# Performance work log

Measured on AMD Instinct MI355X. Metric: run time of the kernel, lower is better.

Reference implementation:

```python
import jax, jax.numpy as jnp
import numpy as np

B, N, C = 8, 8192, 512
H = 8
D = C // H  # 64
EPS = 1e-6


def setup_inputs() -> dict:
    key = jax.random.key(0)
    k1, k2, k3, k4 = jax.random.split(key, 4)
    x = jax.random.normal(k1, (B, N, C), dtype=jnp.float32)
    # nn.Linear(dim, dim*3, bias=False): weight [3C, C]; we store transposed [C, 3C]
    w_qkv = jax.random.normal(k2, (C, 3 * C), dtype=jnp.float32) * (1.0 / np.sqrt(C))
    w_proj = jax.random.normal(k3, (C, C), dtype=jnp.float32) * (1.0 / np.sqrt(C))
    b_proj = jax.random.normal(k4, (C,), dtype=jnp.float32) * 0.01
    return {"x": x, "w_qkv": w_qkv, "w_proj": w_proj, "b_proj": b_proj}


def _linear_attention(q, k, v):
    # q,k,v: [B,H,N,D]; elu+1 feature map, non-causal linear attention
    qf = jax.nn.elu(q) + 1.0
    kf = jax.nn.elu(k) + 1.0
    kv = jnp.einsum('bhnd,bhne->bhde', kf, v)          # [B,H,D,D] state
    z = jnp.einsum('bhnd,bhd->bhn', qf, kf.sum(axis=2))  # normalizer
    out = jnp.einsum('bhnd,bhde->bhne', qf, kv) / (z[..., None] + EPS)
    return out  # [B,H,N,D]


def reference(x, w_qkv, w_proj, b_proj):
    b, n, c = x.shape
    qkv = x @ w_qkv                                   # [B,N,3C]
    qkv = qkv.reshape(b, n, 3, H, D).transpose(2, 0, 3, 1, 4)  # [3,B,H,N,D]
    q, k, v = qkv[0], qkv[1], qkv[2]
    attn = _linear_attention(q, k, v)                 # [B,H,N,D]
    y = attn.transpose(0, 2, 1, 3).reshape(b, n, c)   # [B,N,C]
    return y @ w_proj + b_proj
```

## Files before the change

kernel.cpp:

```cpp
#include <hip/hip_runtime.h>
#include <cstdint>
#include <cstddef>

#define BDIM 8
#define NSEQ 8192
#define CDIM 512
#define HEADS 8
#define HD 64
#define NSPLIT 16

typedef short bf16x8 __attribute__((ext_vector_type(8)));
typedef float f32x4 __attribute__((ext_vector_type(4)));

typedef const __attribute__((address_space(1))) void* gas_cvp;
typedef __attribute__((address_space(3))) void* las_vp;

__device__ __forceinline__ void gload_lds16(const void* g, void* l) {
    __builtin_amdgcn_global_load_lds((gas_cvp)g, (las_vp)l, 16, 0, 0);
}

__device__ __forceinline__ ushort f2bf_rne(float f) {
    uint32_t u = __float_as_uint(f);
    u += 0x7FFFu + ((u >> 16) & 1u);
    return (ushort)(u >> 16);
}
__device__ __forceinline__ float bf2f(ushort h) {
    return __uint_as_float(((uint32_t)h) << 16);
}

__device__ __forceinline__ void split8(const float4 p0, const float4 p1,
                                       bf16x8& hi, bf16x8& lo) {
    const float xs[8] = {p0.x, p0.y, p0.z, p0.w, p1.x, p1.y, p1.z, p1.w};
#pragma unroll
    for (int e = 0; e < 8; ++e) {
        const uint32_t u = __float_as_uint(xs[e]);
        const ushort h = (ushort)(u >> 16);
        const float r = xs[e] - __uint_as_float((uint32_t)h << 16);
        hi[e] = (short)h;
        lo[e] = (short)(__float_as_uint(r) >> 16);
    }
}

__device__ __forceinline__ float elu1(float x) {
    return x > 0.f ? x + 1.f : __expf(x);
}

__global__ __launch_bounds__(256)
void split_wT_kernel(const float* __restrict__ W, ushort* __restrict__ WTh,
                     ushort* __restrict__ WTl, int N) {
    __shared__ float tile[32][33];
    const int tx = threadIdx.x & 31, ty = threadIdx.x >> 5;
    const int bx = blockIdx.x, by = blockIdx.y;
#pragma unroll
    for (int r = 0; r < 4; ++r)
        tile[ty + 8 * r][tx] = W[(size_t)(by * 32 + ty + 8 * r) * N + bx * 32 + tx];
    __syncthreads();
#pragma unroll
    for (int r = 0; r < 4; ++r) {
        const int n = bx * 32 + ty + 8 * r;
        const int k = by * 32 + tx;
        const float v = tile[tx][ty + 8 * r];
        const ushort h = f2bf_rne(v);
        WTh[(size_t)n * 512 + k] = h;
        WTl[(size_t)n * 512 + k] = f2bf_rne(v - bf2f(h));
    }
}

__global__ __launch_bounds__(256, 2)
void qkv_mfma_kernel(const float* __restrict__ X,
                     const ushort* __restrict__ BTh, const ushort* __restrict__ BTl,
                     float* __restrict__ qf, float* __restrict__ kf, float* __restrict__ v) {
    __shared__ __align__(16) char lds[32768];
    const int t = threadIdx.x, l = t & 63, w = t >> 6;
    const int wm = w >> 1, wn = w & 1;
    const int bid = blockIdx.x;
    const int swz = (bid & 7) * 768 + (bid >> 3);
    const int brow = swz / 12, bcol = swz % 12;

    const int f0 = 2 * w, f1 = 2 * w + 1;
    const ushort* gb0 = BTh + (size_t)(bcol * 128 + f0 * 16 + (l & 15)) * 512 + ((l >> 4) * 8);
    const ushort* gb1 = BTh + (size_t)(bcol * 128 + f1 * 16 + (l & 15)) * 512 + ((l >> 4) * 8);
    const ushort* gb2 = BTl + (size_t)(bcol * 128 + f0 * 16 + (l & 15)) * 512 + ((l >> 4) * 8);
    const ushort* gb3 = BTl + (size_t)(bcol * 128 + f1 * 16 + (l & 15)) * 512 + ((l >> 4) * 8);

    const float* gA = X + (size_t)(brow * 128 + wm * 64 + (l & 15)) * 512 + ((l >> 4) * 8);

    f32x4 acc[4][4];
    const f32x4 zero = {0.f, 0.f, 0.f, 0.f};
#pragma unroll
    for (int i = 0; i < 4; ++i)
#pragma unroll
        for (int j = 0; j < 4; ++j) acc[i][j] = zero;

    auto stage = [&](int buf, int kt) {
        char* Ld = lds + buf * 16384;
        gload_lds16(gb0 + kt, Ld + 0 * 8192 + f0 * 1024);
        gload_lds16(gb1 + kt, Ld + 0 * 8192 + f1 * 1024);
        gload_lds16(gb2 + kt, Ld + 1 * 8192 + f0 * 1024);
        gload_lds16(gb3 + kt, Ld + 1 * 8192 + f1 * 1024);
    };

    stage(0, 0);
    __syncthreads();
    int cur = 0;
    for (int ks = 0; ks < 16; ++ks) {
        const int kt = ks * 32;
        if (ks < 15) stage(cur ^ 1, kt + 32);
        bf16x8 ah[4], al[4];
#pragma unroll
        for (int i = 0; i < 4; ++i) {
            const float* pa = gA + (size_t)i * 16 * 512 + kt;
            const float4 p0 = *(const float4*)(pa);
            const float4 p1 = *(const float4*)(pa + 4);
            split8(p0, p1, ah[i], al[i]);
        }
        const char* Lb = lds + cur * 16384;
        bf16x8 bh[4], bl[4];
#pragma unroll
        for (int j = 0; j < 4; ++j) {
            bh[j] = *(const bf16x8*)(Lb + 0 * 8192 + (wn * 4 + j) * 1024 + l * 16);
            bl[j] = *(const bf16x8*)(Lb + 1 * 8192 + (wn * 4 + j) * 1024 + l * 16);
        }
#pragma unroll
        for (int i = 0; i < 4; ++i)
#pragma unroll
            for (int j = 0; j < 4; ++j) {
                acc[i][j] = __builtin_amdgcn_mfma_f32_16x16x32_bf16(ah[i], bh[j], acc[i][j], 0, 0, 0);
                acc[i][j] = __builtin_amdgcn_mfma_f32_16x16x32_bf16(ah[i], bl[j], acc[i][j], 0, 0, 0);
                acc[i][j] = __builtin_amdgcn_mfma_f32_16x16x32_bf16(al[i], bh[j], acc[i][j], 0, 0, 0);
            }
        __syncthreads();
        cur ^= 1;
    }

#pragma unroll
    for (int j = 0; j < 4; ++j) {
        const int gcol = bcol * 128 + wn * 64 + j * 16 + (l & 15);
        const int tt = gcol >> 9;
        const int h  = (gcol >> 6) & 7;
        const int d  = gcol & 63;
        float* dst = (tt == 0) ? qf : (tt == 1) ? kf : v;
#pragma unroll
        for (int i = 0; i < 4; ++i)
#pragma unroll
            for (int r = 0; r < 4; ++r) {
                const int grow = brow * 128 + wm * 64 + i * 16 + (l >> 4) * 4 + r;
                const int b = grow >> 13, n = grow & 8191;
                float val = acc[i][j][r];
                if (tt < 2) val = elu1(val);
                dst[(((size_t)(b * HEADS + h) * NSEQ) + n) * HD + d] = val;
            }
    }
}

__device__ __forceinline__ void mfma3_core(const ushort* __restrict__ Ah,
                                           const ushort* __restrict__ Al,
                                           const ushort* __restrict__ BTh,
                                           const ushort* __restrict__ BTl,
                                           int brow, int bcol, char* lds,
                                           f32x4 acc[4][4]) {
    const int t = threadIdx.x;
    const int l = t & 63;
    const int w = t >> 6;
    const int wm = w >> 1, wn = w & 1;

    const ushort* src = (w == 0) ? Ah : (w == 1) ? Al : (w == 2) ? BTh : BTl;
    const int rowbase = ((w < 2) ? brow : bcol) * 128;
    const ushort* gbase = src + (size_t)(rowbase + (l & 15)) * 512 + ((l >> 4) * 8);

    const f32x4 zero = {0.f, 0.f, 0.f, 0.f};
#pragma unroll
    for (int i = 0; i < 4; ++i)
#pragma unroll
        for (int j = 0; j < 4; ++j) acc[i][j] = zero;

    auto stage = [&](int buf, int kt) {
        const ushort* g = gbase + kt;
        char* ld = lds + buf * 32768 + w * 8192;
#pragma unroll
        for (int f = 0; f < 8; ++f)
            gload_lds16(g + (size_t)f * 16 * 512, ld + f * 1024);
    };

    stage(0, 0);
    __syncthreads();
    int cur = 0;
    for (int ks = 0; ks < 16; ++ks) {
        if (ks < 15) stage(cur ^ 1, (ks + 1) * 32);
        const char* Lb = lds + cur * 32768;
        bf16x8 ah[4], al[4], bh[4], bl[4];
#pragma unroll
        for (int i = 0; i < 4; ++i) {
            ah[i] = *(const bf16x8*)(Lb + 0 * 8192 + (wm * 4 + i) * 1024 + l * 16);
            al[i] = *(const bf16x8*)(Lb + 1 * 8192 + (wm * 4 + i) * 1024 + l * 16);
            bh[i] = *(const bf16x8*)(Lb + 2 * 8192 + (wn * 4 + i) * 1024 + l * 16);
            bl[i] = *(const bf16x8*)(Lb + 3 * 8192 + (wn * 4 + i) * 1024 + l * 16);
        }
#pragma unroll
        for (int i = 0; i < 4; ++i)
#pragma unroll
            for (int j = 0; j < 4; ++j) {
                acc[i][j] = __builtin_amdgcn_mfma_f32_16x16x32_bf16(ah[i], bh[j], acc[i][j], 0, 0, 0);
                acc[i][j] = __builtin_amdgcn_mfma_f32_16x16x32_bf16(ah[i], bl[j], acc[i][j], 0, 0, 0);
                acc[i][j] = __builtin_amdgcn_mfma_f32_16x16x32_bf16(al[i], bh[j], acc[i][j], 0, 0, 0);
            }
        __syncthreads();
        cur ^= 1;
    }
}

__global__ __launch_bounds__(256, 2)
void proj_mfma_kernel(const ushort* __restrict__ Ah, const ushort* __restrict__ Al,
                      const ushort* __restrict__ BTh, const ushort* __restrict__ BTl,
                      const float* __restrict__ bp, float* __restrict__ out) {
    __shared__ __align__(16) char lds[65536];
    const int bid = blockIdx.x;
    const int swz = (bid & 7) * 256 + (bid >> 3);
    const int brow = swz >> 2, bcol = swz & 3;
    f32x4 acc[4][4];
    mfma3_core(Ah, Al, BTh, BTl, brow, bcol, lds, acc);

    const int t = threadIdx.x, l = t & 63, w = t >> 6;
    const int wm = w >> 1, wn = w & 1;
#pragma unroll
    for (int j = 0; j < 4; ++j) {
        const int gcol = bcol * 128 + wn * 64 + j * 16 + (l & 15);
        const float bias = bp[gcol];
#pragma unroll
        for (int i = 0; i < 4; ++i)
#pragma unroll
            for (int r = 0; r < 4; ++r) {
                const int grow = brow * 128 + wm * 64 + i * 16 + (l >> 4) * 4 + r;
                out[(size_t)grow * CDIM + gcol] = acc[i][j][r] + bias;
            }
    }
}

__global__ __launch_bounds__(256, 2)
void kv_state_kernel(const float* __restrict__ kf, const float* __restrict__ v,
                     float* __restrict__ kvpart, float* __restrict__ kspart) {
    __shared__ float kfs[8][64];
    __shared__ float vs[8][64];
    const int t  = threadIdx.x;
    const int s  = blockIdx.x;
    const int bh = blockIdx.y;
    const int d  = t >> 2;
    const int eg = (t & 3) << 4;
    const int ldr = t & 127;
    const int lrow = ldr >> 4;
    const int lseg = (ldr & 15) << 2;
    const float* src = (t < 128) ? (kf + (size_t)bh * NSEQ * HD)
                                 : (v  + (size_t)bh * NSEQ * HD);
    float acc[16];
#pragma unroll
    for (int j = 0; j < 16; j++) acc[j] = 0.f;
    float ks = 0.f;

    const int nbeg = s * (NSEQ / NSPLIT);
    for (int n = nbeg; n < nbeg + (NSEQ / NSPLIT); n += 8) {
        const float4 val = *(const float4*)&src[(size_t)(n + lrow) * HD + lseg];
        __syncthreads();
        if (t < 128) *(float4*)&kfs[lrow][lseg] = val;
        else         *(float4*)&vs[lrow][lseg]  = val;
        __syncthreads();
#pragma unroll
        for (int nn = 0; nn < 8; nn++) {
            const float kval = kfs[nn][d];
            ks += kval;
#pragma unroll
            for (int j = 0; j < 16; j++) acc[j] = fmaf(kval, vs[nn][eg + j], acc[j]);
        }
    }
    float* dst = kvpart + ((size_t)s * 64 + bh) * 4096 + d * 64 + eg;
#pragma unroll
    for (int u = 0; u < 4; u++)
        *(float4*)&dst[u * 4] = make_float4(acc[u*4+0], acc[u*4+1], acc[u*4+2], acc[u*4+3]);
    if ((t & 3) == 0) kspart[((size_t)s * 64 + bh) * 64 + d] = ks;
}

__global__ __launch_bounds__(256, 4)
void kv_reduce_kernel(const float* __restrict__ kvpart, const float* __restrict__ kspart,
                      float* __restrict__ kv, float* __restrict__ ksum) {
    const int idx = blockIdx.x * 256 + threadIdx.x;
    if (blockIdx.x < 1024) {
        float sum = 0.f;
#pragma unroll
        for (int u = 0; u < NSPLIT; u++) sum += kvpart[(size_t)u * 262144 + idx];
        kv[idx] = sum;
    } else {
        const int i2 = idx - 262144;
        float sum = 0.f;
#pragma unroll
        for (int u = 0; u < NSPLIT; u++) sum += kspart[(size_t)u * 4096 + i2];
        ksum[i2] = sum;
    }
}

__global__ __launch_bounds__(256, 2)
void attn_out_kernel(const float* __restrict__ qf, const float* __restrict__ kv,
                     const float* __restrict__ ksum,
                     ushort* __restrict__ yh, ushort* __restrict__ yl) {
    __shared__ float kvl[64][64];
    __shared__ float qfl[64][68];
    __shared__ float ksl[64];
    const int t  = threadIdx.x;
    const int bh = blockIdx.y;
    const int n0 = blockIdx.x * 256;

    const float4* kvg = (const float4*)(kv + (size_t)bh * 4096);
#pragma unroll
    for (int u = 0; u < 4; u++) ((float4*)kvl)[t + u * 256] = kvg[t + u * 256];
    if (t < 64) ksl[t] = ksum[bh * 64 + t];

    const int nl = t >> 2;
    const int eg = (t & 3) << 4;
    const int b = bh >> 3, h = bh & 7;
    const float* qbase = qf + (size_t)bh * NSEQ * HD;

    for (int p = 0; p < 4; p++) {
        const int nb = n0 + p * 64;
        __syncthreads();
        const float4* qg = (const float4*)(qbase + (size_t)nb * HD);
#pragma unroll
        for (int u = 0; u < 4; u++) {
            const int f4 = t + u * 256;
            const int row = f4 >> 4, col = (f4 & 15) << 2;
            *(float4*)&qfl[row][col] = qg[f4];
        }
        __syncthreads();

        float z = 0.f;
#pragma unroll 8
        for (int d = 0; d < 64; ++d) z = fmaf(qfl[nl][d], ksl[d], z);

        float accv[16];
#pragma unroll
        for (int j = 0; j < 16; j++) accv[j] = 0.f;
#pragma unroll 4
        for (int d = 0; d < 64; ++d) {
            const float qv = qfl[nl][d];
#pragma unroll
            for (int j = 0; j < 16; j++) accv[j] = fmaf(qv, kvl[d][eg + j], accv[j]);
        }
        const float inv = 1.f / (z + 1e-6f);
        const size_t rowoff = ((size_t)b * NSEQ + (nb + nl)) * CDIM + h * 64 + eg;
#pragma unroll
        for (int u = 0; u < 4; u++) {
            ushort4 ho, lo4;
            const float o0 = accv[u*4+0]*inv, o1 = accv[u*4+1]*inv,
                        o2 = accv[u*4+2]*inv, o3 = accv[u*4+3]*inv;
            ho.x = f2bf_rne(o0); lo4.x = f2bf_rne(o0 - bf2f(ho.x));
            ho.y = f2bf_rne(o1); lo4.y = f2bf_rne(o1 - bf2f(ho.y));
            ho.z = f2bf_rne(o2); lo4.z = f2bf_rne(o2 - bf2f(ho.z));
            ho.w = f2bf_rne(o3); lo4.w = f2bf_rne(o3 - bf2f(ho.w));
            *(ushort4*)&yh[rowoff + u * 4] = ho;
            *(ushort4*)&yl[rowoff + u * 4] = lo4;
        }
    }
}

extern "C" void kernel_launch(void* const* d_in, const int* in_sizes, int n_in,
                              void* d_out, int out_size, void* d_ws, size_t ws_size,
                              hipStream_t stream) {
    const float* x      = (const float*)d_in[0];
    const float* w_qkv  = (const float*)d_in[1];
    const float* w_proj = (const float*)d_in[2];
    const float* b_proj = (const float*)d_in[3];
    float* out = (float*)d_out;
    char* W = (char*)d_ws;

    float*  qf    = out;
    float*  kf    = (float*)(W);
    ushort* yh    = (ushort*)(W);
    ushort* yl    = (ushort*)(W + 67108864ull);
    float*  vv    = (float*)(W + 134217728ull);
    ushort* wqh   = (ushort*)(W + 268435456ull);
    ushort* wql   = (ushort*)(W + 270008320ull);
    ushort* wph   = (ushort*)(W + 271581184ull);
    ushort* wpl   = (ushort*)(W + 272105472ull);
    float* kvpart = (float*)(W + 272629760ull);
    float* kspart = (float*)(W + 289406976ull);
    float* kv     = (float*)(W + 289669120ull);
    float* ksum   = (float*)(W + 290717696ull);

    split_wT_kernel<<<dim3(48, 16), 256, 0, stream>>>(w_qkv, wqh, wql, 1536);
    split_wT_kernel<<<dim3(16, 16), 256, 0, stream>>>(w_proj, wph, wpl, 512);
    qkv_mfma_kernel<<<6144, 256, 0, stream>>>(x, wqh, wql, qf, kf, vv);
    kv_state_kernel<<<dim3(NSPLIT, 64), 256, 0, stream>>>(kf, vv, kvpart, kspart);
    kv_reduce_kernel<<<1040, 256, 0, stream>>>(kvpart, kspart, kv, ksum);
    attn_out_kernel<<<dim3(32, 64), 256, 0, stream>>>(qf, kv, ksum, yh, yl);
    proj_mfma_kernel<<<2048, 256, 0, stream>>>(yh, yl, wph, wpl, b_proj, out);

    (void)in_sizes; (void)n_in; (void)out_size; (void)ws_size;
}
```

Measured before the change: 1.107 ms.

## Pre-split X into bf16 hi/lo and reuse shared MFMA core for QKV GEMM

Adds a separate pass that converts the fp32 input X into bf16 hi/lo arrays once. The QKV GEMM then stages both operands through LDS with the shared mfma3_core instead of each block re-reading fp32 X from global memory and splitting it in registers. This removes the split work repeated across the 12 column blocks and the uncoalesced direct global loads of A. In exchange it adds an extra kernel that writes 128MB and reads it back, and it reorganises the workspace layout.

```diff
diff --git a/kernel.cpp b/kernel.cpp
--- a/kernel.cpp
+++ b/kernel.cpp
@@ -28,21 +28,22 @@
     return __uint_as_float(((uint32_t)h) << 16);
 }
 
-__device__ __forceinline__ void split8(const float4 p0, const float4 p1,
-                                       bf16x8& hi, bf16x8& lo) {
-    const float xs[8] = {p0.x, p0.y, p0.z, p0.w, p1.x, p1.y, p1.z, p1.w};
-#pragma unroll
-    for (int e = 0; e < 8; ++e) {
-        const uint32_t u = __float_as_uint(xs[e]);
-        const ushort h = (ushort)(u >> 16);
-        const float r = xs[e] - __uint_as_float((uint32_t)h << 16);
-        hi[e] = (short)h;
-        lo[e] = (short)(__float_as_uint(r) >> 16);
-    }
-}
-
 __device__ __forceinline__ float elu1(float x) {
     return x > 0.f ? x + 1.f : __expf(x);
+}
+
+__global__ __launch_bounds__(256)
+void split_x_kernel(const float4* __restrict__ x, ushort4* __restrict__ xh,
+                    ushort4* __restrict__ xl, int n4) {
+    for (int i = blockIdx.x * 256 + threadIdx.x; i < n4; i += gridDim.x * 256) {
+        const float4 v = x[i];
+        ushort4 h, l;
+        h.x = f2bf_rne(v.x); l.x = f2bf_rne(v.x - bf2f(h.x));
+        h.y = f2bf_rne(v.y); l.y = f2bf_rne(v.y - bf2f(h.y));
+        h.z = f2bf_rne(v.z); l.z = f2bf_rne(v.z - bf2f(h.z));
+        h.w = f2bf_rne(v.w); l.w = f2bf_rne(v.w - bf2f(h.w));
+        xh[i] = h; xl[i] = l;
+    }
 }
 
 __global__ __launch_bounds__(256)
@@ -63,93 +64,6 @@
         const ushort h = f2bf_rne(v);
         WTh[(size_t)n * 512 + k] = h;
         WTl[(size_t)n * 512 + k] = f2bf_rne(v - bf2f(h));
-    }
-}
-
-__global__ __launch_bounds__(256, 2)
-void qkv_mfma_kernel(const float* __restrict__ X,
-                     const ushort* __restrict__ BTh, const ushort* __restrict__ BTl,
-                     float* __restrict__ qf, float* __restrict__ kf, float* __restrict__ v) {
-    __shared__ __align__(16) char lds[32768];
-    const int t = threadIdx.x, l = t & 63, w = t >> 6;
-    const int wm = w >> 1, wn = w & 1;
-    const int bid = blockIdx.x;
-    const int swz = (bid & 7) * 768 + (bid >> 3);
-    const int brow = swz / 12, bcol = swz % 12;
-
-    const int f0 = 2 * w, f1 = 2 * w + 1;
-    const ushort* gb0 = BTh + (size_t)(bcol * 128 + f0 * 16 + (l & 15)) * 512 + ((l >> 4) * 8);
-    const ushort* gb1 = BTh + (size_t)(bcol * 128 + f1 * 16 + (l & 15)) * 512 + ((l >> 4) * 8);
-    const ushort* gb2 = BTl + (size_t)(bcol * 128 + f0 * 16 + (l & 15)) * 512 + ((l >> 4) * 8);
-    const ushort* gb3 = BTl + (size_t)(bcol * 128 + f1 * 16 + (l & 15)) * 512 + ((l >> 4) * 8);
-
-    const float* gA = X + (size_t)(brow * 128 + wm * 64 + (l & 15)) * 512 + ((l >> 4) * 8);
-
-    f32x4 acc[4][4];
-    const f32x4 zero = {0.f, 0.f, 0.f, 0.f};
-#pragma unroll
-    for (int i = 0; i < 4; ++i)
-#pragma unroll
-        for (int j = 0; j < 4; ++j) acc[i][j] = zero;
-
-    auto stage = [&](int buf, int kt) {
-        char* Ld = lds + buf * 16384;
-        gload_lds16(gb0 + kt, Ld + 0 * 8192 + f0 * 1024);
-        gload_lds16(gb1 + kt, Ld + 0 * 8192 + f1 * 1024);
-        gload_lds16(gb2 + kt, Ld + 1 * 8192 + f0 * 1024);
-        gload_lds16(gb3 + kt, Ld + 1 * 8192 + f1 * 1024);
-    };
-
-    stage(0, 0);
-    __syncthreads();
-    int cur = 0;
-    for (int ks = 0; ks < 16; ++ks) {
-        const int kt = ks * 32;
-        if (ks < 15) stage(cur ^ 1, kt + 32);
-        bf16x8 ah[4], al[4];
-#pragma unroll
-        for (int i = 0; i < 4; ++i) {
-            const float* pa = gA + (size_t)i * 16 * 512 + kt;
-            const float4 p0 = *(const float4*)(pa);
-            const float4 p1 = *(const float4*)(pa + 4);
-            split8(p0, p1, ah[i], al[i]);
-        }
-        const char* Lb = lds + cur * 16384;
-        bf16x8 bh[4], bl[4];
-#pragma unroll
-        for (int j = 0; j < 4; ++j) {
-            bh[j] = *(const bf16x8*)(Lb + 0 * 8192 + (wn * 4 + j) * 1024 + l * 16);
-            bl[j] = *(const bf16x8*)(Lb + 1 * 8192 + (wn * 4 + j) * 1024 + l * 16);
-        }
-#pragma unroll
-        for (int i = 0; i < 4; ++i)
-#pragma unroll
-            for (int j = 0; j < 4; ++j) {
-                acc[i][j] = __builtin_amdgcn_mfma_f32_16x16x32_bf16(ah[i], bh[j], acc[i][j], 0, 0, 0);
-                acc[i][j] = __builtin_amdgcn_mfma_f32_16x16x32_bf16(ah[i], bl[j], acc[i][j], 0, 0, 0);
-                acc[i][j] = __builtin_amdgcn_mfma_f32_16x16x32_bf16(al[i], bh[j], acc[i][j], 0, 0, 0);
-            }
-        __syncthreads();
-        cur ^= 1;
-    }
-
-#pragma unroll
-    for (int j = 0; j < 4; ++j) {
-        const int gcol = bcol * 128 + wn * 64 + j * 16 + (l & 15);
-        const int tt = gcol >> 9;
-        const int h  = (gcol >> 6) & 7;
-        const int d  = gcol & 63;
-        float* dst = (tt == 0) ? qf : (tt == 1) ? kf : v;
-#pragma unroll
-        for (int i = 0; i < 4; ++i)
-#pragma unroll
-            for (int r = 0; r < 4; ++r) {
-                const int grow = brow * 128 + wm * 64 + i * 16 + (l >> 4) * 4 + r;
-                const int b = grow >> 13, n = grow & 8191;
-                float val = acc[i][j][r];
-                if (tt < 2) val = elu1(val);
-                dst[(((size_t)(b * HEADS + h) * NSEQ) + n) * HD + d] = val;
-            }
     }
 }
 
@@ -206,6 +120,39 @@
             }
         __syncthreads();
         cur ^= 1;
+    }
+}
+
+__global__ __launch_bounds__(256, 2)
+void qkv_mfma_kernel(const ushort* __restrict__ Ah, const ushort* __restrict__ Al,
+                     const ushort* __restrict__ BTh, const ushort* __restrict__ BTl,
+                     float* __restrict__ qf, float* __restrict__ kf, float* __restrict__ v) {
+    __shared__ __align__(16) char lds[65536];
+    const int bid = blockIdx.x;
+    const int swz = (bid & 7) * 768 + (bid >> 3);
+    const int brow = swz / 12, bcol = swz % 12;
+    f32x4 acc[4][4];
+    mfma3_core(Ah, Al, BTh, BTl, brow, bcol, lds, acc);
+
+    const int t = threadIdx.x, l = t & 63, w = t >> 6;
+    const int wm = w >> 1, wn = w & 1;
+#pragma unroll
+    for (int j = 0; j < 4; ++j) {
+        const int gcol = bcol * 128 + wn * 64 + j * 16 + (l & 15);
+        const int tt = gcol >> 9;
+        const int h  = (gcol >> 6) & 7;
+        const int d  = gcol & 63;
+        float* dst = (tt == 0) ? qf : (tt == 1) ? kf : v;
+#pragma unroll
+        for (int i = 0; i < 4; ++i)
+#pragma unroll
+            for (int r = 0; r < 4; ++r) {
+                const int grow = brow * 128 + wm * 64 + i * 16 + (l >> 4) * 4 + r;
+                const int b = grow >> 13, n = grow & 8191;
+                float val = acc[i][j][r];
+                if (tt < 2) val = elu1(val);
+                dst[(((size_t)(b * HEADS + h) * NSEQ) + n) * HD + d] = val;
+            }
     }
 }
 
@@ -370,22 +317,26 @@
     char* W = (char*)d_ws;
 
     float*  qf    = out;
-    float*  kf    = (float*)(W);
-    ushort* yh    = (ushort*)(W);
-    ushort* yl    = (ushort*)(W + 67108864ull);
-    float*  vv    = (float*)(W + 134217728ull);
-    ushort* wqh   = (ushort*)(W + 268435456ull);
-    ushort* wql   = (ushort*)(W + 270008320ull);
-    ushort* wph   = (ushort*)(W + 271581184ull);
-    ushort* wpl   = (ushort*)(W + 272105472ull);
-    float* kvpart = (float*)(W + 272629760ull);
-    float* kspart = (float*)(W + 289406976ull);
-    float* kv     = (float*)(W + 289669120ull);
-    float* ksum   = (float*)(W + 290717696ull);
-
+    ushort* xh    = (ushort*)(W);
+    float*  kvpart= (float*)(W);
+    float*  kspart= (float*)(W + 16777216ull);
+    float*  kv    = (float*)(W + 17039360ull);
+    float*  ksum  = (float*)(W + 18087936ull);
+    ushort* xl    = (ushort*)(W + 67108864ull);
+    float*  kf    = (float*)(W + 134217728ull);
+    ushort* yh    = (ushort*)(W + 134217728ull);
+    ushort* yl    = (ushort*)(W + 201326592ull);
+    float*  vv    = (float*)(W + 268435456ull);
+    ushort* wqh   = (ushort*)(W + 402653184ull);
+    ushort* wql   = (ushort*)(W + 404226048ull);
+    ushort* wph   = (ushort*)(W + 405798912ull);
+    ushort* wpl   = (ushort*)(W + 406323200ull);
+
+    split_x_kernel<<<2048, 256, 0, stream>>>((const float4*)x, (ushort4*)xh,
+                                             (ushort4*)xl, 8388608);
     split_wT_kernel<<<dim3(48, 16), 256, 0, stream>>>(w_qkv, wqh, wql, 1536);
     split_wT_kernel<<<dim3(16, 16), 256, 0, stream>>>(w_proj, wph, wpl, 512);
-    qkv_mfma_kernel<<<6144, 256, 0, stream>>>(x, wqh, wql, qf, kf, vv);
+    qkv_mfma_kernel<<<6144, 256, 0, stream>>>(xh, xl, wqh, wql, qf, kf, vv);
     kv_state_kernel<<<dim3(NSPLIT, 64), 256, 0, stream>>>(kf, vv, kvpart, kspart);
     kv_reduce_kernel<<<1040, 256, 0, stream>>>(kvpart, kspart, kv, ksum);
     attn_out_kernel<<<dim3(32, 64), 256, 0, stream>>>(qf, kv, ksum, yh, yl);
```

After: 1.002 ms. -9.5%, faster.
